# Performance work log

Measured on AMD Instinct MI355X. Metric: run time of the kernel, lower is better.

Reference implementation:

```python
import jax, jax.numpy as jnp
import numpy as np

DT_MIN, DT_MAX, STAB_EPS, RMS_EPS = 1e-4, 10.0, 1e-8, 1e-6


def soft_clamp(x, mn=DT_MIN, mx=DT_MAX):
    center = (mx + mn) / 2.0
    half = (mx - mn) / 2.0
    return center + half * jnp.tanh((x - center) / half)


def setup_inputs() -> dict:
    key = jax.random.key(0)
    ks = jax.random.split(key, 8)
    B, L, D, N = 1, 4096, 1024, 16
    s = D ** -0.5
    x = jax.random.normal(ks[0], (B, L, D), jnp.float32)
    # S4D-real style init: A = -exp(A_log), rows = -(1..N)
    A_log = jnp.broadcast_to(jnp.log(jnp.arange(1, N + 1, dtype=jnp.float32)), (D, N))
    W_delta = jax.random.normal(ks[1], (D, D), jnp.float32) * s
    b_delta = jax.random.normal(ks[2], (D,), jnp.float32) * 0.1
    W_B = jax.random.normal(ks[3], (D, N), jnp.float32) * s
    W_C = jax.random.normal(ks[4], (D, N), jnp.float32) * s
    D_skip = jax.random.normal(ks[5], (D,), jnp.float32) * 0.1 + 1.0
    norm_weight = jnp.ones((D,), jnp.float32)
    return {"x": x, "A_log": A_log, "W_delta": W_delta, "b_delta": b_delta,
            "W_B": W_B, "W_C": W_C, "D_skip": D_skip, "norm_weight": norm_weight}


def reference(x, A_log, W_delta, b_delta, W_B, W_C, D_skip, norm_weight):
    # RMSNorm pre-norm
    rms = jnp.sqrt(jnp.mean(x * x, axis=-1, keepdims=True) + RMS_EPS)
    xn = norm_weight * x / rms                                  # (B, L, D)

    # input-dependent (selective) parameters
    delta = soft_clamp(jax.nn.softplus(xn @ W_delta + b_delta))  # (B, L, D)
    Bp = xn @ W_B                                               # (B, L, N)
    C = xn @ W_C                                                # (B, L, N)
    A = -jnp.exp(A_log)                                         # (D, N)

    # guarded Tustin (bilinear) discretization
    half_dA = 0.5 * delta[..., None] * A                        # (B, L, D, N)
    denom_inv = 1.0 / jnp.maximum(1.0 - half_dA, STAB_EPS)
    A_bar = (1.0 + half_dA) * denom_inv                         # (B, L, D, N)
    B_bar = jnp.sqrt(delta)[..., None] * Bp[:, :, None, :] * denom_inv
    Bx = B_bar * xn[..., None]                                  # (B, L, D, N)

    # linear recurrence h_t = A_bar_t * h_{t-1} + Bx_t ; y_t = sum_n C_t * h_t
    def step(h, inp):
        a_t, bx_t, c_t = inp
        h = a_t * h + bx_t                                      # (B, D, N)
        y_t = jnp.einsum('bdn,bn->bd', h, c_t)
        return h, y_t

    h0 = jnp.zeros((x.shape[0], A.shape[0], A.shape[1]), x.dtype)
    seq = (jnp.moveaxis(A_bar, 1, 0), jnp.moveaxis(Bx, 1, 0), jnp.moveaxis(C, 1, 0))
    _, ys = jax.lax.scan(step, h0, seq)
    y = jnp.moveaxis(ys, 0, 1) + D_skip * xn                    # skip connection
    return y
```

## Files before the change

### kernel.cpp

```cpp
#include <hip/hip_runtime.h>
#include <hip/hip_fp16.h>
#include <cmath>

typedef _Float16 half8 __attribute__((ext_vector_type(8)));
typedef _Float16 half4_t __attribute__((ext_vector_type(4)));
typedef float f32x4 __attribute__((ext_vector_type(4)));

#define LDIM 4096
#define DDIM 1024
#define NSTATE 16
#define NCHUNK 128
#define CLEN 32

#define GLD16(g, l) __builtin_amdgcn_global_load_lds( \
    (const __attribute__((address_space(1))) void*)(g), \
    (__attribute__((address_space(3))) void*)(l), 16, 0, 0)

__global__ __launch_bounds__(256) void k_prep_norm(const float* __restrict__ x,
                                                   const float* __restrict__ nw,
                                                   const float* __restrict__ W,
                                                   const float* __restrict__ WB,
                                                   const float* __restrict__ WC,
                                                   _Float16* __restrict__ xnh,
                                                   _Float16* __restrict__ Wt,
                                                   _Float16* __restrict__ BCe,
                                                   float* __restrict__ bpc) {
  const int b = blockIdx.x, t = threadIdx.x;
  if (b < 4096) {
    const int l = b;
    if (t < 32) bpc[(size_t)l * 32 + t] = 0.f;
    float4 v = ((const float4*)(x + (size_t)l * DDIM))[t];
    float ss = v.x * v.x + v.y * v.y + v.z * v.z + v.w * v.w;
#pragma unroll
    for (int off = 32; off; off >>= 1) ss += __shfl_xor(ss, off, 64);
    __shared__ float sred[4];
    if ((t & 63) == 0) sred[t >> 6] = ss;
    __syncthreads();
    float tot = sred[0] + sred[1] + sred[2] + sred[3];
    float r = rsqrtf(tot * (1.0f / (float)DDIM) + 1e-6f);
    float4 wv = ((const float4*)nw)[t];
    half4_t h;
    h[0] = (_Float16)(v.x * wv.x * r); h[1] = (_Float16)(v.y * wv.y * r);
    h[2] = (_Float16)(v.z * wv.z * r); h[3] = (_Float16)(v.w * wv.w * r);
    ((half4_t*)(xnh + (size_t)l * DDIM))[t] = h;
  } else if (b < 4352) {
    __shared__ float tile[64][65];
    const int bb = b - 4096;
    const int n0 = (bb & 15) * 64, k0 = (bb >> 4) * 64;
#pragma unroll
    for (int i = 0; i < 16; ++i) {
      int idx = t + i * 256;
      int kk = idx >> 6, nn = idx & 63;
      tile[kk][nn] = W[(size_t)(k0 + kk) * DDIM + n0 + nn];
    }
    __syncthreads();
#pragma unroll
    for (int i = 0; i < 16; ++i) {
      int idx = t + i * 256;
      int nn = idx >> 6, kk = idx & 63;
      Wt[(size_t)(n0 + nn) * DDIM + k0 + kk] = (_Float16)tile[kk][nn];
    }
  } else {
    const int by2 = b - 4352;
#pragma unroll
    for (int rr = 0; rr < 2; ++rr) {
      int r = 2 * by2 + rr;
      const float* src = (r & 1) ? WC : WB;
      int n = r >> 1;
#pragma unroll
      for (int j = 0; j < 4; ++j) {
        int k = t * 4 + j;
        BCe[(size_t)r * DDIM + k] = (_Float16)src[(size_t)k * NSTATE + n];
      }
    }
  }
}

__global__ __launch_bounds__(256) void k_gemm128(const _Float16* __restrict__ Ah,
                                                 const _Float16* __restrict__ Bh,
                                                 const _Float16* __restrict__ B2h,
                                                 const float* __restrict__ b_delta,
                                                 _Float16* __restrict__ sdh,
                                                 float* __restrict__ bpc) {
  __shared__ __align__(16) _Float16 As[2][128 * 32];
  __shared__ __align__(16) _Float16 Bs[2][128 * 32];
  __shared__ __align__(16) _Float16 B2s[2][32 * 32];
  const int t = threadIdx.x;
  const int w = t >> 6, lane = t & 63;
  const int quad = lane >> 4, l16 = lane & 15;
  const int wr = w >> 1, wc = w & 1;
  const int bx = blockIdx.x, by = blockIdx.y;
  const int tileM = by * 128, tileN = bx * 128;
  const int srow = lane >> 2, scol = (lane & 3) * 8;
  const _Float16* gA0 = Ah + (size_t)(tileM + w * 32 + srow) * DDIM + scol;
  const _Float16* gB0 = Bh + (size_t)(tileN + w * 32 + srow) * DDIM + scol;
  const _Float16* gC0 = B2h + (size_t)(w * 16 + srow) * DDIM + scol;

  f32x4 acc[4][4], acc2[4];
#pragma unroll
  for (int i = 0; i < 4; ++i) {
    acc2[i] = (f32x4){0.f, 0.f, 0.f, 0.f};
#pragma unroll
    for (int j = 0; j < 4; ++j) acc[i][j] = (f32x4){0.f, 0.f, 0.f, 0.f};
  }

  auto stage = [&](int kt, int p) {
    const int ko = kt * 32;
    GLD16(gA0 + ko,             &As[p][(w * 32) * 32]);
    GLD16(gA0 + 16 * DDIM + ko, &As[p][(w * 32 + 16) * 32]);
    GLD16(gB0 + ko,             &Bs[p][(w * 32) * 32]);
    GLD16(gB0 + 16 * DDIM + ko, &Bs[p][(w * 32 + 16) * 32]);
    if ((kt >> 2) == bx && w < 2)
      GLD16(gC0 + ko,           &B2s[p][(w * 16) * 32]);
  };

  stage(0, 0);
  for (int kt = 0; kt < 32; ++kt) {
    const int p = kt & 1;
    __syncthreads();
    if (kt < 31) stage(kt + 1, p ^ 1);
    half8 af[4], bf[4];
#pragma unroll
    for (int i = 0; i < 4; ++i)
      af[i] = *(const half8*)&As[p][(wr * 64 + i * 16 + l16) * 32 + quad * 8];
#pragma unroll
    for (int j = 0; j < 4; ++j)
      bf[j] = *(const half8*)&Bs[p][(wc * 64 + j * 16 + l16) * 32 + quad * 8];
#pragma unroll
    for (int i = 0; i < 4; ++i)
#pragma unroll
      for (int j = 0; j < 4; ++j)
        acc[i][j] = __builtin_amdgcn_mfma_f32_16x16x32_f16(af[i], bf[j], acc[i][j], 0, 0, 0);
    if ((kt >> 2) == bx) {
      half8 cf = *(const half8*)&B2s[p][(wc * 16 + l16) * 32 + quad * 8];
#pragma unroll
      for (int i = 0; i < 4; ++i)
        acc2[i] = __builtin_amdgcn_mfma_f32_16x16x32_f16(af[i], cf, acc2[i], 0, 0, 0);
    }
  }

  const float cC = 5.00005f, cH = 4.99995f, invH = 1.0f / 4.99995f;
  float bdl[4];
#pragma unroll
  for (int j = 0; j < 4; ++j) bdl[j] = b_delta[tileN + wc * 64 + j * 16 + l16];
#pragma unroll
  for (int i = 0; i < 4; ++i) {
#pragma unroll
    for (int r = 0; r < 4; ++r) {
      int row = tileM + wr * 64 + i * 16 + quad * 4 + r;
#pragma unroll
      for (int j = 0; j < 4; ++j) {
        int col = tileN + wc * 64 + j * 16 + l16;
        float z = acc[i][j][r] + bdl[j];
        float e = __expf(-fabsf(z));
        float sp = fmaxf(z, 0.f) + __logf(1.0f + e);
        float tt = (sp - cC) * invH;
        float e2 = __expf(-2.0f * fabsf(tt));
        float th = copysignf((1.0f - e2) / (1.0f + e2), tt);
        float dt = fmaf(cH, th, cC);
        sdh[(size_t)row * DDIM + col] = (_Float16)sqrtf(dt);
      }
      atomicAdd(&bpc[(size_t)row * 32 + wc * 16 + l16], acc2[i][r]);
    }
  }
}

__global__ __launch_bounds__(256) void k_scan1(const _Float16* __restrict__ sdh,
                                               const _Float16* __restrict__ xnh,
                                               const float* __restrict__ bpc,
                                               const float* __restrict__ A_log,
                                               float2* __restrict__ Ph) {
  __shared__ float2 bcs[CLEN * NSTATE];
  const int t = threadIdx.x;
  const int d = blockIdx.x * 256 + t;
  const int c = blockIdx.y;
#pragma unroll
  for (int u = t; u < CLEN * NSTATE; u += 256) {
    int l = u >> 4, n2 = (u & 15) * 2;
    bcs[u] = *(const float2*)&bpc[(size_t)(c * CLEN + l) * 32 + n2];
  }
  float halfA[NSTATE], h[NSTATE], P[NSTATE];
#pragma unroll
  for (int n = 0; n < NSTATE; ++n) {
    halfA[n] = -0.5f * __expf(A_log[d * NSTATE + n]);
    h[n] = 0.f; P[n] = 1.f;
  }
  __syncthreads();
  const _Float16* sdr = sdh + (size_t)c * CLEN * DDIM + d;
  const _Float16* xr = xnh + (size_t)c * CLEN * DDIM + d;
#pragma unroll 2
  for (int i = 0; i < CLEN; ++i) {
    float sdv = (float)sdr[(size_t)i * DDIM];
    float xv = (float)xr[(size_t)i * DDIM];
    float dsq = sdv * sdv;
    float sdx = sdv * xv;
#pragma unroll
    for (int n = 0; n < NSTATE; ++n) {
      float2 bc = bcs[i * NSTATE + n];
      float hd = dsq * halfA[n];
      float di = __builtin_amdgcn_rcpf(1.0f - hd);
      float ab = fmaf(hd, di, di);
      h[n] = fmaf(ab, h[n], sdx * bc.x * di);
      P[n] *= ab;
    }
  }
#pragma unroll
  for (int n = 0; n < NSTATE; ++n)
    Ph[((size_t)c * NSTATE + n) * DDIM + d] = make_float2(P[n], h[n]);
}

__global__ __launch_bounds__(64) void k_comb(const float2* __restrict__ Ph,
                                             float* __restrict__ Hinit) {
  const int g = blockIdx.x * 64 + threadIdx.x;
  float H = 0.f;
  for (int cb = 0; cb < NCHUNK; cb += 8) {
    float2 ph[8];
#pragma unroll
    for (int u = 0; u < 8; ++u)
      ph[u] = Ph[(size_t)(cb + u) * (DDIM * NSTATE) + g];
#pragma unroll
    for (int u = 0; u < 8; ++u) {
      Hinit[(size_t)(cb + u) * (DDIM * NSTATE) + g] = H;
      H = fmaf(ph[u].x, H, ph[u].y);
    }
  }
}

__global__ __launch_bounds__(256) void k_scan2(const _Float16* __restrict__ sdh,
                                               const _Float16* __restrict__ xnh,
                                               const float* __restrict__ bpc,
                                               const float* __restrict__ A_log,
                                               const float* __restrict__ Hinit,
                                               const float* __restrict__ Dskip,
                                               float* __restrict__ y) {
  __shared__ float2 bcs[CLEN * NSTATE];
  const int t = threadIdx.x;
  const int d = blockIdx.x * 256 + t;
  const int c = blockIdx.y;
#pragma unroll
  for (int u = t; u < CLEN * NSTATE; u += 256) {
    int l = u >> 4, n2 = (u & 15) * 2;
    bcs[u] = *(const float2*)&bpc[(size_t)(c * CLEN + l) * 32 + n2];
  }
  float halfA[NSTATE], h[NSTATE];
#pragma unroll
  for (int n = 0; n < NSTATE; ++n) {
    halfA[n] = -0.5f * __expf(A_log[d * NSTATE + n]);
    h[n] = Hinit[(size_t)c * (DDIM * NSTATE) + n * DDIM + d];
  }
  const float dsk = Dskip[d];
  __syncthreads();
  const _Float16* sdr = sdh + (size_t)c * CLEN * DDIM + d;
  const _Float16* xr = xnh + (size_t)c * CLEN * DDIM + d;
  float* yr = y + (size_t)c * CLEN * DDIM + d;
#pragma unroll 2
  for (int i = 0; i < CLEN; ++i) {
    float sdv = (float)sdr[(size_t)i * DDIM];
    float xv = (float)xr[(size_t)i * DDIM];
    float dsq = sdv * sdv;
    float sdx = sdv * xv;
    float acc = dsk * xv;
#pragma unroll
    for (int n = 0; n < NSTATE; ++n) {
      float2 bc = bcs[i * NSTATE + n];
      float hd = dsq * halfA[n];
      float di = __builtin_amdgcn_rcpf(1.0f - hd);
      float ab = fmaf(hd, di, di);
      h[n] = fmaf(ab, h[n], sdx * bc.x * di);
      acc = fmaf(bc.y, h[n], acc);
    }
    yr[(size_t)i * DDIM] = acc;
  }
}

extern "C" void kernel_launch(void* const* d_in, const int* in_sizes, int n_in,
                              void* d_out, int out_size, void* d_ws, size_t ws_size,
                              hipStream_t stream) {
  const float* x       = (const float*)d_in[0];
  const float* A_log   = (const float*)d_in[1];
  const float* W_delta = (const float*)d_in[2];
  const float* b_delta = (const float*)d_in[3];
  const float* W_B     = (const float*)d_in[4];
  const float* W_C     = (const float*)d_in[5];
  const float* D_skip  = (const float*)d_in[6];
  const float* norm_w  = (const float*)d_in[7];
  float* y = (float*)d_out;

  char* ws = (char*)d_ws;
  const size_t MB = 1024 * 1024;
  _Float16* xnh = (_Float16*)(ws);
  _Float16* Wt  = (_Float16*)(ws + 8 * MB);
  _Float16* BCe = (_Float16*)(ws + 10 * MB);
  _Float16* sdh = (_Float16*)(ws + 11 * MB);
  float*    bpc = (float*)(ws + 19 * MB);
  float2*   Ph  = (float2*)(ws + 20 * MB);
  float*    Hin = (float*)(ws + 36 * MB);
  (void)ws_size; (void)in_sizes; (void)n_in; (void)out_size;

  hipLaunchKernelGGL(k_prep_norm, dim3(4368), dim3(256), 0, stream,
                     x, norm_w, W_delta, W_B, W_C, xnh, Wt, BCe, bpc);
  hipLaunchKernelGGL(k_gemm128, dim3(8, 32), dim3(256), 0, stream,
                     xnh, Wt, BCe, b_delta, sdh, bpc);
  hipLaunchKernelGGL(k_scan1, dim3(4, NCHUNK), dim3(256), 0, stream,
                     sdh, xnh, bpc, A_log, Ph);
  hipLaunchKernelGGL(k_comb, dim3(256), dim3(64), 0, stream, Ph, Hin);
  hipLaunchKernelGGL(k_scan2, dim3(4, NCHUNK), dim3(256), 0, stream,
                     sdh, xnh, bpc, A_log, Hin, D_skip, y);
}
```

Before: 168.7 us.

## Fuse chunked scan passes into one persistent kernel with grid barriers

Replaces the three launches (chunk scan, carry combine, chunk rescan) with a single 512-block kernel that uses two software grid barriers built on atomic counters reset in the prep kernel. Each block keeps its B/C LDS tile and A coefficients across phases, and the combine step runs on 64 blocks of 256 threads instead of 256 blocks of 64. The aim is to remove launch gaps and repeated setup. The trade-off is that correctness depends on all 512 blocks being co-resident (launch bounds request 2 blocks per CU), and 448 blocks sit idle during the serial combine phase.

```diff
diff --git a/kernel.cpp b/kernel.cpp
--- a/kernel.cpp
+++ b/kernel.cpp
@@ -11,10 +11,39 @@
 #define NSTATE 16
 #define NCHUNK 128
 #define CLEN 32
+#define NBLK 512
 
 #define GLD16(g, l) __builtin_amdgcn_global_load_lds( \
     (const __attribute__((address_space(1))) void*)(g), \
     (__attribute__((address_space(3))) void*)(l), 16, 0, 0)
+
+__device__ inline void at_store_f(float* p, float v) {
+  __hip_atomic_store(p, v, __ATOMIC_RELAXED, __HIP_MEMORY_SCOPE_AGENT);
+}
+__device__ inline float at_load_f(const float* p) {
+  return __hip_atomic_load(p, __ATOMIC_RELAXED, __HIP_MEMORY_SCOPE_AGENT);
+}
+__device__ inline void at_store_f2(float2* p, float2 v) {
+  unsigned long long b; __builtin_memcpy(&b, &v, 8);
+  __hip_atomic_store((unsigned long long*)p, b, __ATOMIC_RELAXED, __HIP_MEMORY_SCOPE_AGENT);
+}
+__device__ inline float2 at_load_f2(const float2* p) {
+  unsigned long long b = __hip_atomic_load((const unsigned long long*)p,
+                                           __ATOMIC_RELAXED, __HIP_MEMORY_SCOPE_AGENT);
+  float2 v; __builtin_memcpy(&v, &b, 8); return v;
+}
+
+__device__ inline void gbar(unsigned int* cnt) {
+  __threadfence();
+  __syncthreads();
+  if (threadIdx.x == 0) {
+    __hip_atomic_fetch_add(cnt, 1u, __ATOMIC_ACQ_REL, __HIP_MEMORY_SCOPE_AGENT);
+    while (__hip_atomic_load(cnt, __ATOMIC_ACQUIRE, __HIP_MEMORY_SCOPE_AGENT) < NBLK)
+      __builtin_amdgcn_s_sleep(2);
+  }
+  __syncthreads();
+  __threadfence();
+}
 
 __global__ __launch_bounds__(256) void k_prep_norm(const float* __restrict__ x,
                                                    const float* __restrict__ nw,
@@ -24,7 +53,8 @@
                                                    _Float16* __restrict__ xnh,
                                                    _Float16* __restrict__ Wt,
                                                    _Float16* __restrict__ BCe,
-                                                   float* __restrict__ bpc) {
+                                                   float* __restrict__ bpc,
+                                                   unsigned int* __restrict__ bar) {
   const int b = blockIdx.x, t = threadIdx.x;
   if (b < 4096) {
     const int l = b;
@@ -44,6 +74,7 @@
     h[2] = (_Float16)(v.z * wv.z * r); h[3] = (_Float16)(v.w * wv.w * r);
     ((half4_t*)(xnh + (size_t)l * DDIM))[t] = h;
   } else if (b < 4352) {
+    if (b == 4096 && t < 4) bar[t] = 0u;
     __shared__ float tile[64][65];
     const int bb = b - 4096;
     const int n0 = (bb & 15) * 64, k0 = (bb >> 4) * 64;
@@ -165,15 +196,21 @@
   }
 }
 
-__global__ __launch_bounds__(256) void k_scan1(const _Float16* __restrict__ sdh,
-                                               const _Float16* __restrict__ xnh,
-                                               const float* __restrict__ bpc,
-                                               const float* __restrict__ A_log,
-                                               float2* __restrict__ Ph) {
+__global__ __launch_bounds__(256, 2) void k_scan_fused(const _Float16* __restrict__ sdh,
+                                                       const _Float16* __restrict__ xnh,
+                                                       const float* __restrict__ bpc,
+                                                       const float* __restrict__ A_log,
+                                                       const float* __restrict__ Dskip,
+                                                       float2* __restrict__ Ph,
+                                                       float* __restrict__ Hin,
+                                                       float* __restrict__ y,
+                                                       unsigned int* __restrict__ bar) {
   __shared__ float2 bcs[CLEN * NSTATE];
   const int t = threadIdx.x;
-  const int d = blockIdx.x * 256 + t;
-  const int c = blockIdx.y;
+  const int bid = blockIdx.x;
+  const int dq = bid & 3, c = bid >> 2;
+  const int d = dq * 256 + t;
+
 #pragma unroll
   for (int u = t; u < CLEN * NSTATE; u += 256) {
     int l = u >> 4, n2 = (u & 15) * 2;
@@ -186,90 +223,77 @@
     h[n] = 0.f; P[n] = 1.f;
   }
   __syncthreads();
-  const _Float16* sdr = sdh + (size_t)c * CLEN * DDIM + d;
-  const _Float16* xr = xnh + (size_t)c * CLEN * DDIM + d;
+
+  {
+    const _Float16* sdr = sdh + (size_t)c * CLEN * DDIM + d;
+    const _Float16* xr = xnh + (size_t)c * CLEN * DDIM + d;
 #pragma unroll 2
-  for (int i = 0; i < CLEN; ++i) {
-    float sdv = (float)sdr[(size_t)i * DDIM];
-    float xv = (float)xr[(size_t)i * DDIM];
-    float dsq = sdv * sdv;
-    float sdx = sdv * xv;
-#pragma unroll
-    for (int n = 0; n < NSTATE; ++n) {
-      float2 bc = bcs[i * NSTATE + n];
-      float hd = dsq * halfA[n];
-      float di = __builtin_amdgcn_rcpf(1.0f - hd);
-      float ab = fmaf(hd, di, di);
-      h[n] = fmaf(ab, h[n], sdx * bc.x * di);
-      P[n] *= ab;
-    }
-  }
-#pragma unroll
-  for (int n = 0; n < NSTATE; ++n)
-    Ph[((size_t)c * NSTATE + n) * DDIM + d] = make_float2(P[n], h[n]);
-}
-
-__global__ __launch_bounds__(64) void k_comb(const float2* __restrict__ Ph,
-                                             float* __restrict__ Hinit) {
-  const int g = blockIdx.x * 64 + threadIdx.x;
-  float H = 0.f;
-  for (int cb = 0; cb < NCHUNK; cb += 8) {
-    float2 ph[8];
-#pragma unroll
-    for (int u = 0; u < 8; ++u)
-      ph[u] = Ph[(size_t)(cb + u) * (DDIM * NSTATE) + g];
-#pragma unroll
-    for (int u = 0; u < 8; ++u) {
-      Hinit[(size_t)(cb + u) * (DDIM * NSTATE) + g] = H;
-      H = fmaf(ph[u].x, H, ph[u].y);
-    }
-  }
-}
-
-__global__ __launch_bounds__(256) void k_scan2(const _Float16* __restrict__ sdh,
-                                               const _Float16* __restrict__ xnh,
-                                               const float* __restrict__ bpc,
-                                               const float* __restrict__ A_log,
-                                               const float* __restrict__ Hinit,
-                                               const float* __restrict__ Dskip,
-                                               float* __restrict__ y) {
-  __shared__ float2 bcs[CLEN * NSTATE];
-  const int t = threadIdx.x;
-  const int d = blockIdx.x * 256 + t;
-  const int c = blockIdx.y;
-#pragma unroll
-  for (int u = t; u < CLEN * NSTATE; u += 256) {
-    int l = u >> 4, n2 = (u & 15) * 2;
-    bcs[u] = *(const float2*)&bpc[(size_t)(c * CLEN + l) * 32 + n2];
-  }
-  float halfA[NSTATE], h[NSTATE];
-#pragma unroll
-  for (int n = 0; n < NSTATE; ++n) {
-    halfA[n] = -0.5f * __expf(A_log[d * NSTATE + n]);
-    h[n] = Hinit[(size_t)c * (DDIM * NSTATE) + n * DDIM + d];
-  }
-  const float dsk = Dskip[d];
-  __syncthreads();
-  const _Float16* sdr = sdh + (size_t)c * CLEN * DDIM + d;
-  const _Float16* xr = xnh + (size_t)c * CLEN * DDIM + d;
-  float* yr = y + (size_t)c * CLEN * DDIM + d;
+    for (int i = 0; i < CLEN; ++i) {
+      float sdv = (float)sdr[(size_t)i * DDIM];
+      float xv = (float)xr[(size_t)i * DDIM];
+      float dsq = sdv * sdv;
+      float sdx = sdv * xv;
+#pragma unroll
+      for (int n = 0; n < NSTATE; ++n) {
+        float2 bc = bcs[i * NSTATE + n];
+        float hd = dsq * halfA[n];
+        float di = __builtin_amdgcn_rcpf(1.0f - hd);
+        float ab = fmaf(hd, di, di);
+        h[n] = fmaf(ab, h[n], sdx * bc.x * di);
+        P[n] *= ab;
+      }
+    }
+#pragma unroll
+    for (int n = 0; n < NSTATE; ++n)
+      at_store_f2(&Ph[((size_t)c * NSTATE + n) * DDIM + d], make_float2(P[n], h[n]));
+  }
+
+  gbar(bar + 0);
+
+  if (bid < 64) {
+    const int g = bid * 256 + t;
+    float H = 0.f;
+    for (int cb = 0; cb < NCHUNK; cb += 8) {
+      float2 ph[8];
+#pragma unroll
+      for (int u = 0; u < 8; ++u)
+        ph[u] = at_load_f2(&Ph[(size_t)(cb + u) * (DDIM * NSTATE) + g]);
+#pragma unroll
+      for (int u = 0; u < 8; ++u) {
+        at_store_f(&Hin[(size_t)(cb + u) * (DDIM * NSTATE) + g], H);
+        H = fmaf(ph[u].x, H, ph[u].y);
+      }
+    }
+  }
+
+  gbar(bar + 1);
+
+  {
+#pragma unroll
+    for (int n = 0; n < NSTATE; ++n)
+      h[n] = at_load_f(&Hin[(size_t)c * (DDIM * NSTATE) + n * DDIM + d]);
+    const float dsk = Dskip[d];
+    const _Float16* sdr = sdh + (size_t)c * CLEN * DDIM + d;
+    const _Float16* xr = xnh + (size_t)c * CLEN * DDIM + d;
+    float* yr = y + (size_t)c * CLEN * DDIM + d;
 #pragma unroll 2
-  for (int i = 0; i < CLEN; ++i) {
-    float sdv = (float)sdr[(size_t)i * DDIM];
-    float xv = (float)xr[(size_t)i * DDIM];
-    float dsq = sdv * sdv;
-    float sdx = sdv * xv;
-    float acc = dsk * xv;
-#pragma unroll
-    for (int n = 0; n < NSTATE; ++n) {
-      float2 bc = bcs[i * NSTATE + n];
-      float hd = dsq * halfA[n];
-      float di = __builtin_amdgcn_rcpf(1.0f - hd);
-      float ab = fmaf(hd, di, di);
-      h[n] = fmaf(ab, h[n], sdx * bc.x * di);
-      acc = fmaf(bc.y, h[n], acc);
-    }
-    yr[(size_t)i * DDIM] = acc;
+    for (int i = 0; i < CLEN; ++i) {
+      float sdv = (float)sdr[(size_t)i * DDIM];
+      float xv = (float)xr[(size_t)i * DDIM];
+      float dsq = sdv * sdv;
+      float sdx = sdv * xv;
+      float acc = dsk * xv;
+#pragma unroll
+      for (int n = 0; n < NSTATE; ++n) {
+        float2 bc = bcs[i * NSTATE + n];
+        float hd = dsq * halfA[n];
+        float di = __builtin_amdgcn_rcpf(1.0f - hd);
+        float ab = fmaf(hd, di, di);
+        h[n] = fmaf(ab, h[n], sdx * bc.x * di);
+        acc = fmaf(bc.y, h[n], acc);
+      }
+      yr[(size_t)i * DDIM] = acc;
+    }
   }
 }
 
@@ -295,15 +319,13 @@
   float*    bpc = (float*)(ws + 19 * MB);
   float2*   Ph  = (float2*)(ws + 20 * MB);
   float*    Hin = (float*)(ws + 36 * MB);
+  unsigned int* bar = (unsigned int*)(ws + 44 * MB);
   (void)ws_size; (void)in_sizes; (void)n_in; (void)out_size;
 
   hipLaunchKernelGGL(k_prep_norm, dim3(4368), dim3(256), 0, stream,
-                     x, norm_w, W_delta, W_B, W_C, xnh, Wt, BCe, bpc);
+                     x, norm_w, W_delta, W_B, W_C, xnh, Wt, BCe, bpc, bar);
   hipLaunchKernelGGL(k_gemm128, dim3(8, 32), dim3(256), 0, stream,
                      xnh, Wt, BCe, b_delta, sdh, bpc);
-  hipLaunchKernelGGL(k_scan1, dim3(4, NCHUNK), dim3(256), 0, stream,
-                     sdh, xnh, bpc, A_log, Ph);
-  hipLaunchKernelGGL(k_comb, dim3(256), dim3(64), 0, stream, Ph, Hin);
-  hipLaunchKernelGGL(k_scan2, dim3(4, NCHUNK), dim3(256), 0, stream,
-                     sdh, xnh, bpc, A_log, Hin, D_skip, y);
-}
+  hipLaunchKernelGGL(k_scan_fused, dim3(NBLK), dim3(256), 0, stream,
+                     sdh, xnh, bpc, A_log, D_skip, Ph, Hin, y, bar);
+}
```

New measurement: 553.0 us. +227.8%, slower.
